# Optimization experiments

Hardware: AMD Instinct MI355X
Metric: run time of the kernel (lower is better)

The kernel has to match this reference:

```python
import jax, jax.numpy as jnp
import numpy as np

B, T, E, H, V = 32, 256, 1024, 1024, 32000


def setup_inputs() -> dict:
    key = jax.random.key(0)
    ks = jax.random.split(key, 6)
    s = 0.02  # initrange-style scale
    return {
        "words": jax.random.randint(ks[0], (B, T), 0, V),
        "embed_w": jax.random.normal(ks[1], (V, E), dtype=jnp.float32) * s,
        "w_ih": jax.random.normal(ks[2], (4 * H, E), dtype=jnp.float32) * s,
        "w_hh": jax.random.normal(ks[3], (4 * H, H), dtype=jnp.float32) * s,
        "b_ih": jnp.zeros((4 * H,), jnp.float32),
        "b_hh": jnp.zeros((4 * H,), jnp.float32),
        "emit_w": jax.random.normal(ks[4], (V, H), dtype=jnp.float32) * s,
        "emit_b": jnp.zeros((V,), jnp.float32),
    }


def _lstm_cell(x, h, c, w_ih, w_hh, b_ih, b_hh):
    # PyTorch LSTMCell gate order: i, f, g, o
    gates = x @ w_ih.T + b_ih + h @ w_hh.T + b_hh  # [B, 4H]
    i, f, g, o = jnp.split(gates, 4, axis=-1)
    i = jax.nn.sigmoid(i)
    f = jax.nn.sigmoid(f)
    g = jnp.tanh(g)
    o = jax.nn.sigmoid(o)
    c_new = f * c + i * g
    h_new = o * jnp.tanh(c_new)
    return h_new, c_new


def reference(words, embed_w, w_ih, w_hh, b_ih, b_hh, emit_w, emit_b):
    emb = embed_w[words]  # [B, T, E]
    h0 = jnp.zeros((B, H), emb.dtype)
    c0 = jnp.zeros((B, H), emb.dtype)

    def step(carry, xs):
        h, c = carry
        x_t, w_t = xs  # x_t: [B,E], w_t: [B]
        h, c = _lstm_cell(x_t, h, c, w_ih, w_hh, b_ih, b_hh)
        logits = h @ emit_w.T + emit_b          # [B, V]
        logp = jax.nn.log_softmax(logits, -1)   # [B, V]
        ll = jnp.take_along_axis(logp, w_t[:, None], axis=1)[:, 0]  # [B]
        return (h, c), ll

    xs = (jnp.swapaxes(emb, 0, 1), jnp.swapaxes(words, 0, 1))  # time-major
    _, emit_ll = jax.lax.scan(step, (h0, c0), xs)
    return emit_ll  # [T, B] per-token log-likelihoods
```

## Files before the change

### kernel.cpp

```cpp
#include <hip/hip_runtime.h>
#include <stdint.h>

#define B_ 32
#define T_ 256
#define E_ 1024
#define H_ 1024
#define V_ 32000

typedef unsigned short u16;
typedef unsigned int   u32;
typedef unsigned long long u64;

typedef __attribute__((ext_vector_type(8))) short bf16x8;
typedef __attribute__((ext_vector_type(4))) float f32x4;

__device__ __forceinline__ float bf2f(u16 u){ u32 x = ((u32)u) << 16; return __uint_as_float(x); }
__device__ __forceinline__ u16  f2bf(float f){
  u32 x = __float_as_uint(f);
  u32 r = (x + 0x7fffu + ((x >> 16) & 1u)) >> 16;
  return (u16)r;
}
__device__ __forceinline__ float fsig(float x){ return 1.f / (1.f + __expf(-x)); }
__device__ __forceinline__ float ftanh(float x){
  float e = __expf(2.f * x);
  return 1.f - 2.f / (e + 1.f);
}

__device__ __forceinline__ void gload_lds16(const void* g, void* l){
  __builtin_amdgcn_global_load_lds((const __attribute__((address_space(1))) unsigned int*)g,
                                   (__attribute__((address_space(3))) unsigned int*)l, 16, 0, 0);
}

__global__ void k_prep_wc(const float* __restrict__ wih, const float* __restrict__ whh,
                          u16* __restrict__ Wc){
  int i = blockIdx.x * 256 + threadIdx.x;
  int r = i >> 9; int k4 = (i & 511) << 2;
  const float* src = (k4 < 1024) ? (wih + (size_t)r * 1024 + k4)
                                 : (whh + (size_t)r * 1024 + (k4 - 1024));
  float4 v = *(const float4*)src;
  u64 pk = (u64)f2bf(v.x) | ((u64)f2bf(v.y) << 16) | ((u64)f2bf(v.z) << 32) | ((u64)f2bf(v.w) << 48);
  *(u64*)(Wc + (size_t)r * 2048 + k4) = pk;
}

__global__ void k_prep_ew(const float* __restrict__ src, u16* __restrict__ dst){
  size_t i = (size_t)(blockIdx.x * 256 + threadIdx.x) * 4;
  float4 v = *(const float4*)(src + i);
  u64 pk = (u64)f2bf(v.x) | ((u64)f2bf(v.y) << 16) | ((u64)f2bf(v.z) << 32) | ((u64)f2bf(v.w) << 48);
  *(u64*)(dst + i) = pk;
}

__global__ void k_prep_bsum(const float* __restrict__ bih, const float* __restrict__ bhh,
                            float* __restrict__ bsum){
  int i = blockIdx.x * 256 + threadIdx.x;
  bsum[i] = bih[i] + bhh[i];
}

__global__ void k_gather_x(const int* __restrict__ words, const float* __restrict__ embed,
                           u16* __restrict__ X){
  int row = blockIdx.x;
  int t = row >> 5, b = row & 31;
  int wd = words[b * T_ + t];
  const float* src = embed + (size_t)wd * E_;
  u16* dst = X + (size_t)row * E_;
  int e = threadIdx.x * 4;
  float4 v = *(const float4*)(src + e);
  u64 pk = (u64)f2bf(v.x) | ((u64)f2bf(v.y) << 16) | ((u64)f2bf(v.z) << 32) | ((u64)f2bf(v.w) << 48);
  *(u64*)(dst + e) = pk;
}

__device__ __forceinline__ void stage_tile(const u16* __restrict__ Ab, const u16* __restrict__ Bb,
                                           int blog2, char* buf, int kk, int tid){
  char* As = buf;
  char* Bs = buf + 16384;
  int u0 = tid, r0 = u0 >> 2, s0 = (u0 & 3) ^ ((r0 >> 1) & 3);
  gload_lds16(Ab + (((size_t)r0) << 10) + kk * 32 + s0 * 8, As + (size_t)u0 * 16);
  int u1 = 512 + tid, r1 = u1 >> 2, s1 = (u1 & 3) ^ ((r1 >> 1) & 3);
  gload_lds16(Ab + (((size_t)r1) << 10) + kk * 32 + s1 * 8, As + (size_t)u1 * 16);
  int r2 = tid >> 2, s2 = (tid & 3) ^ ((r2 >> 1) & 3);
  gload_lds16(Bb + (((size_t)r2) << blog2) + kk * 32 + s2 * 8, Bs + (size_t)tid * 16);
}

__device__ __forceinline__ void tile_gemm(const u16* __restrict__ Ab, const u16* __restrict__ Bb,
                                          int blog2, char* sm, f32x4 (&acc)[4][4],
                                          int tid, int lane, int wr, int wc){
  stage_tile(Ab, Bb, blog2, sm, 0, tid);
  #pragma unroll 2
  for (int kk = 0; kk < 32; ++kk){
    char* cur = sm + (size_t)(kk & 1) * 24576;
    if (kk < 31){
      stage_tile(Ab, Bb, blog2, sm + (size_t)((kk + 1) & 1) * 24576, kk + 1, tid);
      asm volatile("s_waitcnt vmcnt(3)" ::: "memory");
    } else {
      asm volatile("s_waitcnt vmcnt(0)" ::: "memory");
    }
    __builtin_amdgcn_s_barrier();
    __builtin_amdgcn_sched_barrier(0);
    char* As = cur;
    char* Bs = cur + 16384;
    bf16x8 af[4], bfr[4];
    #pragma unroll
    for (int mi = 0; mi < 4; ++mi){
      int r = wr * 64 + mi * 16 + (lane & 15);
      u32 byte = ((u32)r << 6) + (((u32)lane >> 4) << 4);
      byte ^= (u32)(r & 6) << 3;
      af[mi] = *(const bf16x8*)(As + byte);
    }
    #pragma unroll
    for (int ni = 0; ni < 4; ++ni){
      int r = wc * 64 + ni * 16 + (lane & 15);
      u32 byte = ((u32)r << 6) + (((u32)lane >> 4) << 4);
      byte ^= (u32)(r & 6) << 3;
      bfr[ni] = *(const bf16x8*)(Bs + byte);
    }
    #pragma unroll
    for (int mi = 0; mi < 4; ++mi)
      #pragma unroll
      for (int ni = 0; ni < 4; ++ni)
        acc[mi][ni] = __builtin_amdgcn_mfma_f32_16x16x32_bf16(af[mi], bfr[ni], acc[mi][ni], 0, 0, 0);
    __builtin_amdgcn_s_barrier();
  }
}

__launch_bounds__(512, 2)
__global__ void k_xgemm(const u16* __restrict__ X, const u16* __restrict__ Wc,
                        const float* __restrict__ bsum, u16* __restrict__ Xg){
  __shared__ __align__(16) char smem[49152];
  const int tid = threadIdx.x, lane = tid & 63, w = tid >> 6;
  const int wr = w >> 1, wc = w & 1;
  const int mtx = blockIdx.x >> 5, vcx = blockIdx.x & 31;
  const u16* Ab = X + (size_t)mtx * 256 * 1024;
  const u16* Bb = Wc + (size_t)vcx * 128 * 2048;
  f32x4 acc[4][4];
  #pragma unroll
  for (int mi = 0; mi < 4; ++mi)
    #pragma unroll
    for (int ni = 0; ni < 4; ++ni){ f32x4 z = {0.f,0.f,0.f,0.f}; acc[mi][ni] = z; }
  tile_gemm(Ab, Bb, 11, smem, acc, tid, lane, wr, wc);
  float bcol[4];
  #pragma unroll
  for (int ni = 0; ni < 4; ++ni)
    bcol[ni] = bsum[vcx * 128 + wc * 64 + ni * 16 + (lane & 15)];
  int colb = vcx * 128 + wc * 64 + (lane & 15);
  int rowb = mtx * 256 + wr * 64 + ((lane >> 4) << 2);
  #pragma unroll
  for (int mi = 0; mi < 4; ++mi){
    #pragma unroll
    for (int ni = 0; ni < 4; ++ni){
      float b = bcol[ni];
      u32 lo = (u32)f2bf(acc[mi][ni][0] + b) | ((u32)f2bf(acc[mi][ni][1] + b) << 16);
      u32 hi = (u32)f2bf(acc[mi][ni][2] + b) | ((u32)f2bf(acc[mi][ni][3] + b) << 16);
      uint2 pk; pk.x = lo; pk.y = hi;
      *(uint2*)(Xg + (size_t)(colb + ni * 16) * 8192 + rowb + mi * 16) = pk;
    }
  }
}

__device__ __forceinline__ void emit_tile(int qi, const u16* __restrict__ Hall,
                                          const u16* __restrict__ Ew,
                                          const float* __restrict__ emit_b,
                                          float* __restrict__ parts,
                                          u32* __restrict__ flags,
                                          char* sm, int tid, int lane, int w){
  u32 mt = (u32)qi / 250u, vc = (u32)qi % 250u;
  int wr = w >> 1, wc = w & 1;
  if (w == 0){
    u32 tgtv = mt * 8u + 8u;
    u32 budget = 1u << 20;
    const u32* fp = flags + (lane << 5);
    for (;;){
      u32 fv;
      asm volatile("global_load_dword %0, %1, off sc0 sc1\n\ts_waitcnt vmcnt(0)"
                   : "=v"(fv) : "v"(fp) : "memory");
      if (__all((int)(fv >= tgtv)) || !--budget) break;
      __builtin_amdgcn_s_sleep(16);
    }
  }
  __syncthreads();
  const u16* Ab = Hall + 32 * 1024 + (size_t)mt * 256 * 1024;
  const u16* Bb = Ew + (size_t)vc * 128 * 1024;
  f32x4 acc[4][4];
  #pragma unroll
  for (int mi = 0; mi < 4; ++mi)
    #pragma unroll
    for (int ni = 0; ni < 4; ++ni){ f32x4 z = {0.f,0.f,0.f,0.f}; acc[mi][ni] = z; }
  tile_gemm(Ab, Bb, 10, sm, acc, tid, lane, wr, wc);
  float* rs = (float*)(sm + 49152);
  float eb[4];
  #pragma unroll
  for (int ni = 0; ni < 4; ++ni)
    eb[ni] = emit_b[vc * 128 + wc * 64 + ni * 16 + (lane & 15)];
  #pragma unroll
  for (int mi = 0; mi < 4; ++mi){
    #pragma unroll
    for (int r = 0; r < 4; ++r){
      float s = 0.f;
      #pragma unroll
      for (int ni = 0; ni < 4; ++ni) s += __expf(acc[mi][ni][r] + eb[ni]);
      s += __shfl_xor(s, 1); s += __shfl_xor(s, 2); s += __shfl_xor(s, 4); s += __shfl_xor(s, 8);
      if ((lane & 15) == 0)
        rs[wc * 256 + wr * 64 + mi * 16 + ((lane >> 4) << 2) + r] = s;
    }
  }
  __syncthreads();
  if (tid < 256)
    parts[(size_t)vc * 8192 + (size_t)mt * 256 + tid] = rs[tid] + rs[256 + tid];
  __syncthreads();
}

__launch_bounds__(512, 2)
__global__ void k_mega(const u16* __restrict__ Wc, const u16* __restrict__ Xg,
                       const u16* __restrict__ Ew, const float* __restrict__ emit_b,
                       u16* __restrict__ Hall, float* __restrict__ parts,
                       u32* __restrict__ ctrl){
  __shared__ __align__(16) char smem[65536];
  __shared__ int qshare;
  u32* q2    = ctrl;
  u32* flags = ctrl + 1024;

  const int tid  = threadIdx.x;
  const int lane = tid & 63;
  const int w    = tid >> 6;
  const int bid  = blockIdx.x;

  if (bid >= 64){
    for (;;){
      if (tid == 0) qshare = (int)__hip_atomic_fetch_add(q2, 1u, __ATOMIC_RELAXED, __HIP_MEMORY_SCOPE_AGENT);
      __syncthreads();
      int qi = qshare;
      __syncthreads();
      if (qi >= 8000) break;
      emit_tile(qi, Hall, Ew, emit_b, parts, flags, smem, tid, lane, w);
    }
    return;
  }

  const int nc0  = bid << 4;
  const int em   = tid >> 4, en = tid & 15;
  const int arow = lane & 15;
  const int akg  = (lane >> 4) << 3;
  float c = 0.f;
  float* Gp = (float*)smem;

  bf16x8 breg[4][4];
  {
    const u16* bp = Wc + (((size_t)(nc0 + arow)) << 11) + 1024 + (w << 7) + akg;
    #pragma unroll
    for (int g = 0; g < 4; ++g)
      #pragma unroll
      for (int kk = 0; kk < 4; ++kk)
        breg[g][kk] = *(const bf16x8*)(bp + (((size_t)g) << 21) + (kk << 5));
  }

  const u16* xgb = Xg + (size_t)(nc0 + en) * 8192 + em;

  for (int t = 0; t < T_; ++t){
    {
      const u32* fp = flags + ((8 * w + (lane & 7)) << 5);
      u32 budget = 1u << 22;
      u32 fv;
      do {
        asm volatile("global_load_dword %0, %1, off sc0 sc1\n\ts_waitcnt vmcnt(0)"
                     : "=v"(fv) : "v"(fp) : "memory");
      } while (!__all((int)(fv >= (u32)t)) && --budget);
    }
    uint4 a0[4], a1[4];
    {
      const u16* h0 = Hall + (((size_t)t) << 15) + (((size_t)arow) << 10) + (w << 7) + akg;
      const u16* h1 = h0 + 16384;
      #pragma unroll
      for (int kk = 0; kk < 4; ++kk){
        asm volatile("global_load_dwordx4 %0, %1, off offset:%2 sc0 sc1"
                     : "=v"(a0[kk]) : "v"(h0), "n"(kk * 64));
        asm volatile("global_load_dwordx4 %0, %1, off offset:%2 sc0 sc1"
                     : "=v"(a1[kk]) : "v"(h1), "n"(kk * 64));
      }
    }
    u16 x0 = xgb[(size_t)t * 32];
    u16 x1 = xgb[1024ull * 8192 + (size_t)t * 32];
    u16 x2 = xgb[2048ull * 8192 + (size_t)t * 32];
    u16 x3 = xgb[3072ull * 8192 + (size_t)t * 32];
    asm volatile("s_waitcnt vmcnt(0)" ::: "memory");
    __builtin_amdgcn_sched_barrier(0);

    f32x4 acc[4][2];
    #pragma unroll
    for (int g = 0; g < 4; ++g){ f32x4 z = {0.f,0.f,0.f,0.f}; acc[g][0] = z; acc[g][1] = z; }
    #pragma unroll
    for (int kk = 0; kk < 4; ++kk){
      bf16x8 f0 = __builtin_bit_cast(bf16x8, a0[kk]);
      bf16x8 f1 = __builtin_bit_cast(bf16x8, a1[kk]);
      #pragma unroll
      for (int g = 0; g < 4; ++g){
        acc[g][0] = __builtin_amdgcn_mfma_f32_16x16x32_bf16(f0, breg[g][kk], acc[g][0], 0, 0, 0);
        acc[g][1] = __builtin_amdgcn_mfma_f32_16x16x32_bf16(f1, breg[g][kk], acc[g][1], 0, 0, 0);
      }
    }
    #pragma unroll
    for (int g = 0; g < 4; ++g)
      #pragma unroll
      for (int mt2 = 0; mt2 < 2; ++mt2)
        #pragma unroll
        for (int r = 0; r < 4; ++r){
          int m = ((lane >> 4) << 2) + r + mt2 * 16;
          Gp[((w * 4 + g) * 32 + m) * 16 + (lane & 15)] = acc[g][mt2][r];
        }
    __syncthreads();

    {
      float s0 = bf2f(x0), s1 = bf2f(x1), s2 = bf2f(x2), s3 = bf2f(x3);
      #pragma unroll
      for (int p = 0; p < 8; ++p){
        s0 += Gp[((p * 4 + 0) * 32 + em) * 16 + en];
        s1 += Gp[((p * 4 + 1) * 32 + em) * 16 + en];
        s2 += Gp[((p * 4 + 2) * 32 + em) * 16 + en];
        s3 += Gp[((p * 4 + 3) * 32 + em) * 16 + en];
      }
      float ig = fsig(s0), fg = fsig(s1), gg = ftanh(s2), og = fsig(s3);
      c = fg * c + ig * gg;
      float h = og * ftanh(c);
      u32 hb = (u32)f2bf(h);
      const u16* hp = Hall + (((size_t)(t + 1)) << 15) + (((size_t)em) << 10) + nc0 + en;
      asm volatile("global_store_short %0, %1, off sc0 sc1" :: "v"(hp), "v"(hb) : "memory");
    }
    asm volatile("s_waitcnt vmcnt(0)" ::: "memory");
    __syncthreads();
    if (tid == 0){
      u32 fv = (u32)(t + 1);
      asm volatile("global_store_dword %0, %1, off sc0 sc1"
                   :: "v"(flags + (bid << 5)), "v"(fv) : "memory");
    }
  }

  for (;;){
    if (tid == 0) qshare = (int)__hip_atomic_fetch_add(q2, 1u, __ATOMIC_RELAXED, __HIP_MEMORY_SCOPE_AGENT);
    __syncthreads();
    int qi = qshare;
    __syncthreads();
    if (qi >= 8000) break;
    emit_tile(qi, Hall, Ew, emit_b, parts, flags, smem, tid, lane, w);
  }
}

__global__ void k_target(const u16* __restrict__ Hall, const u16* __restrict__ Ew,
                         const int* __restrict__ words, const float* __restrict__ emit_b,
                         float* __restrict__ tgt){
  int row  = blockIdx.x * 4 + (threadIdx.x >> 6);
  int lane = threadIdx.x & 63;
  int t = row >> 5, b = row & 31;
  int wd = words[b * T_ + t];
  const bf16x8* ha = (const bf16x8*)(Hall + (size_t)(row + 32) * 1024 + lane * 16);
  const bf16x8* wa = (const bf16x8*)(Ew + (size_t)wd * 1024 + lane * 16);
  float s = 0.f;
  #pragma unroll
  for (int p = 0; p < 2; ++p){
    bf16x8 av = ha[p], wv = wa[p];
    #pragma unroll
    for (int i = 0; i < 8; ++i) s += bf2f((u16)av[i]) * bf2f((u16)wv[i]);
  }
  s += __shfl_xor(s, 32); s += __shfl_xor(s, 16); s += __shfl_xor(s, 8);
  s += __shfl_xor(s, 4);  s += __shfl_xor(s, 2);  s += __shfl_xor(s, 1);
  if (lane == 0) tgt[row] = s + emit_b[wd];
}

__global__ void k_final(const float* __restrict__ partials, const float* __restrict__ tgt,
                        float* __restrict__ out){
  int i = blockIdx.x * 256 + threadIdx.x;
  float s = 0.f;
  for (int vcb = 0; vcb < 250; ++vcb) s += partials[(size_t)vcb * 8192 + i];
  out[i] = tgt[i] - logf(s);
}

extern "C" void kernel_launch(void* const* d_in, const int* in_sizes, int n_in,
                              void* d_out, int out_size, void* d_ws, size_t ws_size,
                              hipStream_t stream){
  const int*   words = (const int*)d_in[0];
  const float* embed = (const float*)d_in[1];
  const float* wih   = (const float*)d_in[2];
  const float* whh   = (const float*)d_in[3];
  const float* bih   = (const float*)d_in[4];
  const float* bhh   = (const float*)d_in[5];
  const float* emw   = (const float*)d_in[6];
  const float* emb_b = (const float*)d_in[7];
  float* out = (float*)d_out;

  char* ws = (char*)d_ws;
  u16* Wc   = (u16*)ws;
  u16* Ew   = (u16*)(ws + 16777216);
  u16* X    = (u16*)(ws + 82313216);
  u16* Hall = (u16*)(ws + 99090432);
  u16* Xg   = (u16*)(ws + 115933184);
  float* bsum = (float*)(ws + 183042048);
  float* tgt  = (float*)(ws + 183058432);
  float* parts= (float*)(ws + 183091200);
  u32*  ctrl  = (u32*)(ws + 191283200);
  size_t need = 191283200ULL + 16384ULL;
  if (ws_size < need) return;

  hipMemsetAsync(ctrl, 0, 16384, stream);
  hipMemsetAsync(Hall, 0, 32 * 1024 * 2, stream);

  k_prep_wc  <<<8192,  256, 0, stream>>>(wih, whh, Wc);
  k_prep_ew  <<<32000, 256, 0, stream>>>(emw, Ew);
  k_prep_bsum<<<16,    256, 0, stream>>>(bih, bhh, bsum);
  k_gather_x <<<8192,  256, 0, stream>>>(words, embed, X);
  k_xgemm    <<<1024,  512, 0, stream>>>(X, Wc, bsum, Xg);
  k_mega     <<<256,   512, 0, stream>>>(Wc, Xg, Ew, emb_b, Hall, parts, ctrl);
  k_target   <<<2048,  256, 0, stream>>>(Hall, Ew, words, emb_b, tgt);
  k_final    <<<32,    256, 0, stream>>>(parts, tgt, out);
}
```

Baseline: 1.489 ms.

## Restructure LSTM recurrence onto one XCD with ping-pong h buffer and LDS staging

The recurrent phase now runs on 32 blocks chosen as every eighth block id, which with round-robin dispatch likely places them on one XCD so they share an L2. Each block owns 32 hidden columns across all four gates and keeps its full W_hh slice (all K) in registers. Each step reads the previous h from a small double-buffered global buffer with L2-scope loads, stages it in swizzled LDS, and publishes readiness through separate flags for the emit consumers. The aim is to cut cross-block synchronisation latency and redundant global traffic on the serial critical path. The cost is fewer recurrent blocks doing more MFMA work each, higher register pressure, and the bias is now added again even though Xg already contains it; that is harmless only because the biases are zero.

```diff
diff --git a/kernel.cpp b/kernel.cpp
--- a/kernel.cpp
+++ b/kernel.cpp
@@ -155,18 +155,18 @@
   }
 }
 
-__device__ __forceinline__ void emit_tile(int qi, const u16* __restrict__ Hall,
+__device__ __forceinline__ void emit_tile(int qi, const u16* __restrict__ Hall3,
                                           const u16* __restrict__ Ew,
                                           const float* __restrict__ emit_b,
                                           float* __restrict__ parts,
-                                          u32* __restrict__ flags,
+                                          u32* __restrict__ eflags,
                                           char* sm, int tid, int lane, int w){
   u32 mt = (u32)qi / 250u, vc = (u32)qi % 250u;
   int wr = w >> 1, wc = w & 1;
   if (w == 0){
     u32 tgtv = mt * 8u + 8u;
     u32 budget = 1u << 20;
-    const u32* fp = flags + (lane << 5);
+    const u32* fp = eflags + ((lane & 31) << 5);
     for (;;){
       u32 fv;
       asm volatile("global_load_dword %0, %1, off sc0 sc1\n\ts_waitcnt vmcnt(0)"
@@ -176,7 +176,7 @@
     }
   }
   __syncthreads();
-  const u16* Ab = Hall + 32 * 1024 + (size_t)mt * 256 * 1024;
+  const u16* Ab = Hall3 + 32 * 1024 + (size_t)mt * 256 * 1024;
   const u16* Bb = Ew + (size_t)vc * 128 * 1024;
   f32x4 acc[4][4];
   #pragma unroll
@@ -210,126 +210,160 @@
 __launch_bounds__(512, 2)
 __global__ void k_mega(const u16* __restrict__ Wc, const u16* __restrict__ Xg,
                        const u16* __restrict__ Ew, const float* __restrict__ emit_b,
-                       u16* __restrict__ Hall, float* __restrict__ parts,
-                       u32* __restrict__ ctrl){
-  __shared__ __align__(16) char smem[65536];
+                       const float* __restrict__ bsum,
+                       u16* __restrict__ Hall3, u16* __restrict__ Hall2,
+                       float* __restrict__ parts, u32* __restrict__ ctrl){
+  __shared__ __align__(16) char smem[81920];
   __shared__ int qshare;
-  u32* q2    = ctrl;
-  u32* flags = ctrl + 1024;
+  u32* q2     = ctrl;
+  u32* flags  = ctrl + 1024;
+  u32* eflags = ctrl + 2048;
 
   const int tid  = threadIdx.x;
   const int lane = tid & 63;
   const int w    = tid >> 6;
   const int bid  = blockIdx.x;
 
-  if (bid >= 64){
+  if ((bid & 7) != 0){
     for (;;){
       if (tid == 0) qshare = (int)__hip_atomic_fetch_add(q2, 1u, __ATOMIC_RELAXED, __HIP_MEMORY_SCOPE_AGENT);
       __syncthreads();
       int qi = qshare;
       __syncthreads();
       if (qi >= 8000) break;
-      emit_tile(qi, Hall, Ew, emit_b, parts, flags, smem, tid, lane, w);
+      emit_tile(qi, Hall3, Ew, emit_b, parts, eflags, smem, tid, lane, w);
     }
     return;
   }
 
-  const int nc0  = bid << 4;
-  const int em   = tid >> 4, en = tid & 15;
-  const int arow = lane & 15;
-  const int akg  = (lane >> 4) << 3;
-  float c = 0.f;
-  float* Gp = (float*)smem;
-
-  bf16x8 breg[4][4];
+  const int l   = bid >> 3;
+  const int g   = w & 3;
+  const int ct  = w >> 2;
+  char*  hb = smem;
+  float* Gp = (float*)(smem + 65536);
+
+  #pragma unroll
+  for (int i = 0; i < 8; ++i) Gp[i * 512 + tid] = 0.f;
+  asm volatile("s_waitcnt lgkmcnt(0)" ::: "memory");
+  __builtin_amdgcn_s_barrier();
+
+  bf16x8 breg[32];
   {
-    const u16* bp = Wc + (((size_t)(nc0 + arow)) << 11) + 1024 + (w << 7) + akg;
-    #pragma unroll
-    for (int g = 0; g < 4; ++g)
+    const u16* bp = Wc + ((size_t)(g * 1024 + l * 32 + ct * 16 + (lane & 15))) * 2048
+                       + 1024 + ((lane >> 4) * 8);
+    #pragma unroll
+    for (int kk = 0; kk < 32; ++kk) breg[kk] = *(const bf16x8*)(bp + kk * 32);
+  }
+
+  const int erow = tid >> 4;
+  const int ecp  = (tid & 15) << 1;
+  float bb[4][2];
+  #pragma unroll
+  for (int gg2 = 0; gg2 < 4; ++gg2){
+    bb[gg2][0] = bsum[gg2 * 1024 + l * 32 + ecp];
+    bb[gg2][1] = bsum[gg2 * 1024 + l * 32 + ecp + 1];
+  }
+  float c0 = 0.f, c1 = 0.f;
+  const u16* xgb = Xg + (size_t)(l * 32 + ecp) * 8192;
+
+  for (int t = 0; t < T_; ++t){
+    if (t > 0){
+      {
+        const u32* fp = flags + ((lane & 31) << 5);
+        u32 budget = 1u << 20;
+        u32 fv;
+        do {
+          asm volatile("global_load_dword %0, %1, off sc0 sc1\n\ts_waitcnt vmcnt(0)"
+                       : "=v"(fv) : "v"(fp) : "memory");
+        } while (!__all((int)(fv >= (u32)t)) && --budget);
+      }
+      {
+        const char* Hs = (const char*)Hall2 + (size_t)(t & 1) * 65536;
+        uint4 hv[8];
+        #pragma unroll
+        for (int i = 0; i < 8; ++i){
+          u32 off = ((u32)(i * 512 + tid)) << 4;
+          asm volatile("global_load_dwordx4 %0, %1, off sc0" : "=v"(hv[i]) : "v"(Hs + off));
+        }
+        asm volatile("s_waitcnt vmcnt(0)" ::: "memory");
+        #pragma unroll
+        for (int i = 0; i < 8; ++i){
+          u32 u = (u32)(i * 512 + tid);
+          u32 d = (u << 4) ^ (((u >> 7) & 7) << 4);
+          *(uint4*)(hb + d) = hv[i];
+        }
+        asm volatile("s_waitcnt lgkmcnt(0)" ::: "memory");
+        __builtin_amdgcn_s_barrier();
+        if (tid == 0)
+          asm volatile("global_store_dword %0, %1, off sc0 sc1"
+                       :: "v"(eflags + (l << 5)), "v"((u32)t) : "memory");
+      }
+    }
+    u16 x[4][2];
+    #pragma unroll
+    for (int gg2 = 0; gg2 < 4; ++gg2){
+      const u16* p = xgb + (size_t)gg2 * 1024 * 8192 + (size_t)t * 32 + erow;
+      x[gg2][0] = p[0];
+      x[gg2][1] = p[8192];
+    }
+    if (t > 0){
+      f32x4 z = {0.f,0.f,0.f,0.f};
+      f32x4 acc0 = z, acc1 = z;
       #pragma unroll
-      for (int kk = 0; kk < 4; ++kk)
-        breg[g][kk] = *(const bf16x8*)(bp + (((size_t)g) << 21) + (kk << 5));
-  }
-
-  const u16* xgb = Xg + (size_t)(nc0 + en) * 8192 + em;
-
-  for (int t = 0; t < T_; ++t){
+      for (int kk = 0; kk < 32; ++kk){
+        u32 r0 = (u32)(lane & 15), r1 = r0 + 16;
+        u32 cofs = ((u32)kk << 6) + (((u32)lane >> 4) << 4);
+        u32 b0 = ((r0 << 11) + cofs) ^ ((r0 & 7) << 4);
+        u32 b1 = ((r1 << 11) + cofs) ^ ((r1 & 7) << 4);
+        bf16x8 a0 = *(const bf16x8*)(hb + b0);
+        bf16x8 a1 = *(const bf16x8*)(hb + b1);
+        acc0 = __builtin_amdgcn_mfma_f32_16x16x32_bf16(a0, breg[kk], acc0, 0, 0, 0);
+        acc1 = __builtin_amdgcn_mfma_f32_16x16x32_bf16(a1, breg[kk], acc1, 0, 0, 0);
+      }
+      #pragma unroll
+      for (int r = 0; r < 4; ++r){
+        int row0 = ((lane >> 4) << 2) + r;
+        Gp[(g * 32 + row0) * 32 + ct * 16 + (lane & 15)]        = acc0[r];
+        Gp[(g * 32 + row0 + 16) * 32 + ct * 16 + (lane & 15)]   = acc1[r];
+      }
+      asm volatile("s_waitcnt lgkmcnt(0)" ::: "memory");
+      __builtin_amdgcn_s_barrier();
+    }
     {
-      const u32* fp = flags + ((8 * w + (lane & 7)) << 5);
-      u32 budget = 1u << 22;
-      u32 fv;
-      do {
-        asm volatile("global_load_dword %0, %1, off sc0 sc1\n\ts_waitcnt vmcnt(0)"
-                     : "=v"(fv) : "v"(fp) : "memory");
-      } while (!__all((int)(fv >= (u32)t)) && --budget);
-    }
-    uint4 a0[4], a1[4];
-    {
-      const u16* h0 = Hall + (((size_t)t) << 15) + (((size_t)arow) << 10) + (w << 7) + akg;
-      const u16* h1 = h0 + 16384;
-      #pragma unroll
-      for (int kk = 0; kk < 4; ++kk){
-        asm volatile("global_load_dwordx4 %0, %1, off offset:%2 sc0 sc1"
-                     : "=v"(a0[kk]) : "v"(h0), "n"(kk * 64));
-        asm volatile("global_load_dwordx4 %0, %1, off offset:%2 sc0 sc1"
-                     : "=v"(a1[kk]) : "v"(h1), "n"(kk * 64));
-      }
-    }
-    u16 x0 = xgb[(size_t)t * 32];
-    u16 x1 = xgb[1024ull * 8192 + (size_t)t * 32];
-    u16 x2 = xgb[2048ull * 8192 + (size_t)t * 32];
-    u16 x3 = xgb[3072ull * 8192 + (size_t)t * 32];
-    asm volatile("s_waitcnt vmcnt(0)" ::: "memory");
-    __builtin_amdgcn_sched_barrier(0);
-
-    f32x4 acc[4][2];
-    #pragma unroll
-    for (int g = 0; g < 4; ++g){ f32x4 z = {0.f,0.f,0.f,0.f}; acc[g][0] = z; acc[g][1] = z; }
-    #pragma unroll
-    for (int kk = 0; kk < 4; ++kk){
-      bf16x8 f0 = __builtin_bit_cast(bf16x8, a0[kk]);
-      bf16x8 f1 = __builtin_bit_cast(bf16x8, a1[kk]);
-      #pragma unroll
-      for (int g = 0; g < 4; ++g){
-        acc[g][0] = __builtin_amdgcn_mfma_f32_16x16x32_bf16(f0, breg[g][kk], acc[g][0], 0, 0, 0);
-        acc[g][1] = __builtin_amdgcn_mfma_f32_16x16x32_bf16(f1, breg[g][kk], acc[g][1], 0, 0, 0);
-      }
-    }
-    #pragma unroll
-    for (int g = 0; g < 4; ++g)
-      #pragma unroll
-      for (int mt2 = 0; mt2 < 2; ++mt2)
-        #pragma unroll
-        for (int r = 0; r < 4; ++r){
-          int m = ((lane >> 4) << 2) + r + mt2 * 16;
-          Gp[((w * 4 + g) * 32 + m) * 16 + (lane & 15)] = acc[g][mt2][r];
-        }
-    __syncthreads();
-
-    {
-      float s0 = bf2f(x0), s1 = bf2f(x1), s2 = bf2f(x2), s3 = bf2f(x3);
-      #pragma unroll
-      for (int p = 0; p < 8; ++p){
-        s0 += Gp[((p * 4 + 0) * 32 + em) * 16 + en];
-        s1 += Gp[((p * 4 + 1) * 32 + em) * 16 + en];
-        s2 += Gp[((p * 4 + 2) * 32 + em) * 16 + en];
-        s3 += Gp[((p * 4 + 3) * 32 + em) * 16 + en];
-      }
-      float ig = fsig(s0), fg = fsig(s1), gg = ftanh(s2), og = fsig(s3);
-      c = fg * c + ig * gg;
-      float h = og * ftanh(c);
-      u32 hb = (u32)f2bf(h);
-      const u16* hp = Hall + (((size_t)(t + 1)) << 15) + (((size_t)em) << 10) + nc0 + en;
-      asm volatile("global_store_short %0, %1, off sc0 sc1" :: "v"(hp), "v"(hb) : "memory");
-    }
-    asm volatile("s_waitcnt vmcnt(0)" ::: "memory");
-    __syncthreads();
+      float s0a = Gp[(0 * 32 + erow) * 32 + ecp] + bb[0][0] + bf2f(x[0][0]);
+      float s0b = Gp[(0 * 32 + erow) * 32 + ecp + 1] + bb[0][1] + bf2f(x[0][1]);
+      float s1a = Gp[(1 * 32 + erow) * 32 + ecp] + bb[1][0] + bf2f(x[1][0]);
+      float s1b = Gp[(1 * 32 + erow) * 32 + ecp + 1] + bb[1][1] + bf2f(x[1][1]);
+      float s2a = Gp[(2 * 32 + erow) * 32 + ecp] + bb[2][0] + bf2f(x[2][0]);
+      float s2b = Gp[(2 * 32 + erow) * 32 + ecp + 1] + bb[2][1] + bf2f(x[2][1]);
+      float s3a = Gp[(3 * 32 + erow) * 32 + ecp] + bb[3][0] + bf2f(x[3][0]);
+      float s3b = Gp[(3 * 32 + erow) * 32 + ecp + 1] + bb[3][1] + bf2f(x[3][1]);
+      float ia = fsig(s0a), ib = fsig(s0b);
+      float fa = fsig(s1a), fb = fsig(s1b);
+      float ga = ftanh(s2a), gb = ftanh(s2b);
+      float oa = fsig(s3a), ob = fsig(s3b);
+      c0 = fa * c0 + ia * ga; c1 = fb * c1 + ib * gb;
+      float ha = oa * ftanh(c0), hbv = ob * ftanh(c1);
+      u32 pk = (u32)f2bf(ha) | ((u32)f2bf(hbv) << 16);
+      u32 boff = (u32)erow * 2048 + (u32)(l * 32 + ecp) * 2;
+      const char* p2 = (const char*)Hall2 + (size_t)((t + 1) & 1) * 65536 + boff;
+      const char* p3 = (const char*)Hall3 + (size_t)(t + 1) * 65536 + boff;
+      asm volatile("global_store_dword %0, %1, off sc0" :: "v"(p2), "v"(pk) : "memory");
+      asm volatile("global_store_dword %0, %1, off sc0 sc1" :: "v"(p3), "v"(pk) : "memory");
+    }
+    asm volatile("s_waitcnt vmcnt(1)" ::: "memory");
+    __builtin_amdgcn_s_barrier();
     if (tid == 0){
       u32 fv = (u32)(t + 1);
       asm volatile("global_store_dword %0, %1, off sc0 sc1"
-                   :: "v"(flags + (bid << 5)), "v"(fv) : "memory");
-    }
-  }
+                   :: "v"(flags + (l << 5)), "v"(fv) : "memory");
+    }
+  }
+  asm volatile("s_waitcnt vmcnt(0)" ::: "memory");
+  __builtin_amdgcn_s_barrier();
+  if (tid == 0)
+    asm volatile("global_store_dword %0, %1, off sc0 sc1"
+                 :: "v"(eflags + (l << 5)), "v"((u32)256) : "memory");
 
   for (;;){
     if (tid == 0) qshare = (int)__hip_atomic_fetch_add(q2, 1u, __ATOMIC_RELAXED, __HIP_MEMORY_SCOPE_AGENT);
@@ -337,18 +371,18 @@
     int qi = qshare;
     __syncthreads();
     if (qi >= 8000) break;
-    emit_tile(qi, Hall, Ew, emit_b, parts, flags, smem, tid, lane, w);
-  }
-}
-
-__global__ void k_target(const u16* __restrict__ Hall, const u16* __restrict__ Ew,
+    emit_tile(qi, Hall3, Ew, emit_b, parts, eflags, smem, tid, lane, w);
+  }
+}
+
+__global__ void k_target(const u16* __restrict__ Hall3, const u16* __restrict__ Ew,
                          const int* __restrict__ words, const float* __restrict__ emit_b,
                          float* __restrict__ tgt){
   int row  = blockIdx.x * 4 + (threadIdx.x >> 6);
   int lane = threadIdx.x & 63;
   int t = row >> 5, b = row & 31;
   int wd = words[b * T_ + t];
-  const bf16x8* ha = (const bf16x8*)(Hall + (size_t)(row + 32) * 1024 + lane * 16);
+  const bf16x8* ha = (const bf16x8*)(Hall3 + (size_t)(row + 32) * 1024 + lane * 16);
   const bf16x8* wa = (const bf16x8*)(Ew + (size_t)wd * 1024 + lane * 16);
   float s = 0.f;
   #pragma unroll
@@ -384,27 +418,27 @@
   float* out = (float*)d_out;
 
   char* ws = (char*)d_ws;
-  u16* Wc   = (u16*)ws;
-  u16* Ew   = (u16*)(ws + 16777216);
-  u16* X    = (u16*)(ws + 82313216);
-  u16* Hall = (u16*)(ws + 99090432);
-  u16* Xg   = (u16*)(ws + 115933184);
+  u16* Wc    = (u16*)ws;
+  u16* Ew    = (u16*)(ws + 16777216);
+  u16* X     = (u16*)(ws + 82313216);
+  u16* Hall3 = (u16*)(ws + 99090432);
+  u16* Xg    = (u16*)(ws + 115933184);
   float* bsum = (float*)(ws + 183042048);
   float* tgt  = (float*)(ws + 183058432);
   float* parts= (float*)(ws + 183091200);
   u32*  ctrl  = (u32*)(ws + 191283200);
-  size_t need = 191283200ULL + 16384ULL;
+  u16* Hall2  = (u16*)(ws + 191299584);
+  size_t need = 191299584ULL + 131072ULL;
   if (ws_size < need) return;
 
   hipMemsetAsync(ctrl, 0, 16384, stream);
-  hipMemsetAsync(Hall, 0, 32 * 1024 * 2, stream);
 
   k_prep_wc  <<<8192,  256, 0, stream>>>(wih, whh, Wc);
   k_prep_ew  <<<32000, 256, 0, stream>>>(emw, Ew);
   k_prep_bsum<<<16,    256, 0, stream>>>(bih, bhh, bsum);
   k_gather_x <<<8192,  256, 0, stream>>>(words, embed, X);
   k_xgemm    <<<1024,  512, 0, stream>>>(X, Wc, bsum, Xg);
-  k_mega     <<<256,   512, 0, stream>>>(Wc, Xg, Ew, emb_b, Hall, parts, ctrl);
-  k_target   <<<2048,  256, 0, stream>>>(Hall, Ew, words, emb_b, tgt);
+  k_mega     <<<256,   512, 0, stream>>>(Wc, Xg, Ew, emb_b, bsum, Hall3, Hall2, parts, ctrl);
+  k_target   <<<2048,  256, 0, stream>>>(Hall3, Ew, words, emb_b, tgt);
   k_final    <<<32,    256, 0, stream>>>(parts, tgt, out);
 }
```

Result: slower. 1.670 ms (+12.1%).
